# Kernel optimization log

Hardware: AMD Instinct MI355X
Metric: run time of the kernel (lower is better)

## Reference

```python
import jax, jax.numpy as jnp
import numpy as np

V = 6          # veldim
U = 4          # lstm_units
SEQLEN = 64
N = 1920 * 1080  # pixels in Lsx/Lsy


def setup_inputs() -> dict:
    key = jax.random.key(0)
    ks = jax.random.split(key, 24)
    f = lambda i, shape, s=0.1: jax.random.normal(ks[i], shape, jnp.float32) * s
    inp = {
        'vel': f(0, (V,), 1.0),
        'Lsx': jax.random.normal(ks[1], (N, V), jnp.float32),
        'Lsy': jax.random.normal(ks[2], (N, V), jnp.float32),
        # parameters (torch.Tensor uninitialized -> we use small randn)
        'Wix': f(3, (V, U)), 'Wih': f(4, (V * U, U)), 'bi': f(5, (V, U)),
        'Wfx': f(6, (V, U)), 'Wfh': f(7, (V * U, U)), 'bf': f(8, (V, U)),
        'Wox': f(9, (V, U)), 'Woh': f(10, (V * U, U)), 'bo': f(11, (V, U)),
        'Wgx': f(12, (V, U)), 'Wgh': f(13, (V * U, U)), 'bg': f(14, (V, U)),
        'linear': f(15, (V, U)), 'bl': f(16, (V,)),
        # initial hidden/cell state (torch.randn in init_hidden)
        'h0': jax.random.normal(ks[17], (V, U), jnp.float32),
        'c0': jax.random.normal(ks[18], (V, U), jnp.float32),
    }
    return inp


def reference(vel, Lsx, Lsy, Wix, Wih, bi, Wfx, Wfh, bf,
              Wox, Woh, bo, Wgx, Wgh, bg, linear, bl, h0, c0):
    def step(x, h, c):
        xv = x.reshape(V, 1)  # broadcast column, as x.view(6,1)
        # torch: sum(W * (R @ h), dim=1).view(V,U); row 4j+u of R@h is h[j]
        # => gate_h[j,u] = dot(W[4j+u,:], h[j,:])
        def gh(W):
            return jnp.einsum('juk,jk->ju', W.reshape(V, U, U), h)
        it = jax.nn.sigmoid(Wix * xv + gh(Wih) + bi)
        ft = jax.nn.sigmoid(Wfx * xv + gh(Wfh) + bf)
        ot = jax.nn.sigmoid(Wox * xv + gh(Woh) + bo)
        cbar = jax.nn.sigmoid(Wgx * xv + gh(Wgh) + bg)  # sigmoid, as in source
        c2 = ft * c + it * cbar
        h2 = ot * jax.nn.sigmoid(c2)  # sigmoid (not tanh), as in source
        out = jnp.tanh(jnp.sum(linear * h2, axis=1) + bl)  # (V,)
        return out, h2, c2

    out, h, c = step(vel, h0, c0)
    vels = out  # i == 0 branch

    # i = 1 .. seqlen-1: vels += previous out, then advance the cell.
    def body(carry, _):
        h, c, out, vels = carry
        vels = vels + out
        out, h, c = step(out, h, c)
        return (h, c, out, vels), None

    (h, c, out, vels), _ = jax.lax.scan(body, (h, c, out, vels), None,
                                        length=SEQLEN - 1)

    # f_hat = cat(sum(Lsx*vels,-1), sum(Lsy*vels,-1)) -> (N, 2)
    fx = Lsx @ vels
    fy = Lsy @ vels
    return jnp.stack([fx, fy], axis=-1)
```

## Files before the change

### kernel.cpp

```cpp
#include <hip/hip_runtime.h>
#include <hip/hip_bf16.h>


#define V 6
#define U 4
#define SEQLEN 64

__device__ __forceinline__ float sigm(float x) {
    return 1.0f / (1.0f + __expf(-x));
}
__device__ __forceinline__ float tanh_f(float x) {
    float e = __expf(2.0f * x);
    return 1.0f - 2.0f / (e + 1.0f);
}

template <int CTRL>
__device__ __forceinline__ float qp(float x) {
    return __int_as_float(
        __builtin_amdgcn_mov_dpp(__float_as_int(x), CTRL, 0xF, 0xF, true));
}

__global__ void lstm_vels_kernel(
    const float* __restrict__ vel,
    const float* __restrict__ Wix, const float* __restrict__ Wih, const float* __restrict__ bi,
    const float* __restrict__ Wfx, const float* __restrict__ Wfh, const float* __restrict__ bf_,
    const float* __restrict__ Wox, const float* __restrict__ Woh, const float* __restrict__ bo,
    const float* __restrict__ Wgx, const float* __restrict__ Wgh, const float* __restrict__ bg,
    const float* __restrict__ lin, const float* __restrict__ bl,
    const float* __restrict__ h0,  const float* __restrict__ c0,
    float* __restrict__ vels_out)
{
    const int lane = threadIdx.x;
    if (lane >= V * U) return;
    const int j  = lane >> 2;
    const int u  = lane & 3;
    const int r4 = lane * 4;

    const float wix = Wix[lane], bii = bi[lane];
    const float wfx = Wfx[lane], bff = bf_[lane];
    const float wox = Wox[lane], boo = bo[lane];
    const float wgx = Wgx[lane], bgg = bg[lane];
    const float li  = lin[lane];
    const float blj = bl[j];

    const int k1 = u ^ 1, k2 = u ^ 2, k3 = u ^ 3;
    const float wi0 = Wih[r4 + u],  wi1 = Wih[r4 + k1];
    const float wi2 = Wih[r4 + k2], wi3 = Wih[r4 + k3];
    const float wf0 = Wfh[r4 + u],  wf1 = Wfh[r4 + k1];
    const float wf2 = Wfh[r4 + k2], wf3 = Wfh[r4 + k3];
    const float wo0 = Woh[r4 + u],  wo1 = Woh[r4 + k1];
    const float wo2 = Woh[r4 + k2], wo3 = Woh[r4 + k3];
    const float wg0 = Wgh[r4 + u],  wg1 = Wgh[r4 + k1];
    const float wg2 = Wgh[r4 + k2], wg3 = Wgh[r4 + k3];

    float h = h0[lane];
    float c = c0[lane];
    float x = vel[j];

    float vels = 0.0f, o = 0.0f;

    for (int i = 0; i < SEQLEN; ++i) {
        if (i > 0) { vels += o; x = o; }

        const float hA = qp<0xB1>(h);
        const float hB = qp<0x4E>(h);
        const float hC = qp<0x4E>(hA);

        float pi = fmaf(wix, x, bii);
        pi = fmaf(wi0, h, pi); pi = fmaf(wi1, hA, pi);
        pi = fmaf(wi2, hB, pi); pi = fmaf(wi3, hC, pi);
        float pf = fmaf(wfx, x, bff);
        pf = fmaf(wf0, h, pf); pf = fmaf(wf1, hA, pf);
        pf = fmaf(wf2, hB, pf); pf = fmaf(wf3, hC, pf);
        float po = fmaf(wox, x, boo);
        po = fmaf(wo0, h, po); po = fmaf(wo1, hA, po);
        po = fmaf(wo2, hB, po); po = fmaf(wo3, hC, po);
        float pg = fmaf(wgx, x, bgg);
        pg = fmaf(wg0, h, pg); pg = fmaf(wg1, hA, pg);
        pg = fmaf(wg2, hB, pg); pg = fmaf(wg3, hC, pg);

        const float it = sigm(pi);
        const float ft = sigm(pf);
        const float ot = sigm(po);
        const float gt = sigm(pg);

        c = fmaf(ft, c, it * gt);
        h = ot * sigm(c);

        float s = li * h;
        s += qp<0xB1>(s);
        s += qp<0x4E>(s);
        o = tanh_f(s + blj);

        if (i == 0) vels = o;
    }

    if (u == 0) vels_out[j] = vels;
}

__global__ __launch_bounds__(256) void flow_kernel(
    const float* __restrict__ Lsx, const float* __restrict__ Lsy,
    const float* __restrict__ velsp, float* __restrict__ out, int n)
{
    const int t = blockIdx.x * blockDim.x + threadIdx.x;

    float v[6];
#pragma unroll
    for (int k = 0; k < 6; ++k) v[k] = velsp[k];

    const int p0 = t * 2;
    if (p0 + 1 < n) {
        const float4* ax = reinterpret_cast<const float4*>(Lsx + (size_t)p0 * 6);
        const float4* ay = reinterpret_cast<const float4*>(Lsy + (size_t)p0 * 6);
        union { float4 q[3]; float s[12]; } bx, by;
        bx.q[0] = ax[0]; bx.q[1] = ax[1]; bx.q[2] = ax[2];
        by.q[0] = ay[0]; by.q[1] = ay[1]; by.q[2] = ay[2];

        float4 r;
        float fx0 = 0.0f, fy0 = 0.0f, fx1 = 0.0f, fy1 = 0.0f;
#pragma unroll
        for (int k = 0; k < 6; ++k) {
            fx0 = fmaf(bx.s[k],     v[k], fx0);
            fy0 = fmaf(by.s[k],     v[k], fy0);
            fx1 = fmaf(bx.s[6 + k], v[k], fx1);
            fy1 = fmaf(by.s[6 + k], v[k], fy1);
        }
        r.x = fx0; r.y = fy0; r.z = fx1; r.w = fy1;
        reinterpret_cast<float4*>(out)[t] = r;
    } else {
        for (int p = p0; p < n; ++p) {
            float fx = 0.0f, fy = 0.0f;
            for (int k = 0; k < 6; ++k) {
                fx = fmaf(Lsx[(size_t)p * 6 + k], v[k], fx);
                fy = fmaf(Lsy[(size_t)p * 6 + k], v[k], fy);
            }
            out[2 * p]     = fx;
            out[2 * p + 1] = fy;
        }
    }
}

extern "C" void kernel_launch(void* const* d_in, const int* in_sizes, int n_in,
                              void* d_out, int out_size, void* d_ws, size_t ws_size,
                              hipStream_t stream)
{
    const float* vel  = (const float*)d_in[0];
    const float* Lsx  = (const float*)d_in[1];
    const float* Lsy  = (const float*)d_in[2];
    const float* Wix  = (const float*)d_in[3];
    const float* Wih  = (const float*)d_in[4];
    const float* bi   = (const float*)d_in[5];
    const float* Wfx  = (const float*)d_in[6];
    const float* Wfh  = (const float*)d_in[7];
    const float* bf_  = (const float*)d_in[8];
    const float* Wox  = (const float*)d_in[9];
    const float* Woh  = (const float*)d_in[10];
    const float* bo   = (const float*)d_in[11];
    const float* Wgx  = (const float*)d_in[12];
    const float* Wgh  = (const float*)d_in[13];
    const float* bg   = (const float*)d_in[14];
    const float* lin  = (const float*)d_in[15];
    const float* bl   = (const float*)d_in[16];
    const float* h0   = (const float*)d_in[17];
    const float* c0   = (const float*)d_in[18];

    float* vels = (float*)d_ws;
    const int n = in_sizes[1] / V;

    lstm_vels_kernel<<<1, 64, 0, stream>>>(vel, Wix, Wih, bi, Wfx, Wfh, bf_,
                                           Wox, Woh, bo, Wgx, Wgh, bg,
                                           lin, bl, h0, c0, vels);

    const int nt = (n + 1) / 2;
    flow_kernel<<<(nt + 255) / 256, 256, 0, stream>>>(Lsx, Lsy, vels,
                                                      (float*)d_out, n);
}
```

Measured before the change: 176.7 us.

## Fuse LSTM recurrence into flow kernel with grid-stride loop

```diff
diff --git a/kernel.cpp b/kernel.cpp
--- a/kernel.cpp
+++ b/kernel.cpp
@@ -20,7 +20,7 @@
         __builtin_amdgcn_mov_dpp(__float_as_int(x), CTRL, 0xF, 0xF, true));
 }
 
-__global__ void lstm_vels_kernel(
+__global__ __launch_bounds__(256, 4) void fused_lstm_flow_kernel(
     const float* __restrict__ vel,
     const float* __restrict__ Wix, const float* __restrict__ Wih, const float* __restrict__ bi,
     const float* __restrict__ Wfx, const float* __restrict__ Wfh, const float* __restrict__ bf_,
@@ -28,115 +28,122 @@
     const float* __restrict__ Wgx, const float* __restrict__ Wgh, const float* __restrict__ bg,
     const float* __restrict__ lin, const float* __restrict__ bl,
     const float* __restrict__ h0,  const float* __restrict__ c0,
-    float* __restrict__ vels_out)
+    const float* __restrict__ Lsx, const float* __restrict__ Lsy,
+    float* __restrict__ out, int n)
 {
-    const int lane = threadIdx.x;
-    if (lane >= V * U) return;
-    const int j  = lane >> 2;
-    const int u  = lane & 3;
-    const int r4 = lane * 4;
+    __shared__ float vels_s[8];
 
-    const float wix = Wix[lane], bii = bi[lane];
-    const float wfx = Wfx[lane], bff = bf_[lane];
-    const float wox = Wox[lane], boo = bo[lane];
-    const float wgx = Wgx[lane], bgg = bg[lane];
-    const float li  = lin[lane];
-    const float blj = bl[j];
+    if (threadIdx.x < 24) {
+        const int lane = threadIdx.x;
+        const int j  = lane >> 2;
+        const int u  = lane & 3;
+        const int r4 = lane * 4;
 
-    const int k1 = u ^ 1, k2 = u ^ 2, k3 = u ^ 3;
-    const float wi0 = Wih[r4 + u],  wi1 = Wih[r4 + k1];
-    const float wi2 = Wih[r4 + k2], wi3 = Wih[r4 + k3];
-    const float wf0 = Wfh[r4 + u],  wf1 = Wfh[r4 + k1];
-    const float wf2 = Wfh[r4 + k2], wf3 = Wfh[r4 + k3];
-    const float wo0 = Woh[r4 + u],  wo1 = Woh[r4 + k1];
-    const float wo2 = Woh[r4 + k2], wo3 = Woh[r4 + k3];
-    const float wg0 = Wgh[r4 + u],  wg1 = Wgh[r4 + k1];
-    const float wg2 = Wgh[r4 + k2], wg3 = Wgh[r4 + k3];
+        const float wix = Wix[lane], bii = bi[lane];
+        const float wfx = Wfx[lane], bff = bf_[lane];
+        const float wox = Wox[lane], boo = bo[lane];
+        const float wgx = Wgx[lane], bgg = bg[lane];
+        const float li  = lin[lane];
+        const float blj = bl[j];
 
-    float h = h0[lane];
-    float c = c0[lane];
-    float x = vel[j];
+        const int k1 = u ^ 1, k2 = u ^ 2, k3 = u ^ 3;
+        const float wi0 = Wih[r4 + u],  wi1 = Wih[r4 + k1];
+        const float wi2 = Wih[r4 + k2], wi3 = Wih[r4 + k3];
+        const float wf0 = Wfh[r4 + u],  wf1 = Wfh[r4 + k1];
+        const float wf2 = Wfh[r4 + k2], wf3 = Wfh[r4 + k3];
+        const float wo0 = Woh[r4 + u],  wo1 = Woh[r4 + k1];
+        const float wo2 = Woh[r4 + k2], wo3 = Woh[r4 + k3];
+        const float wg0 = Wgh[r4 + u],  wg1 = Wgh[r4 + k1];
+        const float wg2 = Wgh[r4 + k2], wg3 = Wgh[r4 + k3];
 
-    float vels = 0.0f, o = 0.0f;
+        float h = h0[lane];
+        float c = c0[lane];
+        float x = vel[j];
 
-    for (int i = 0; i < SEQLEN; ++i) {
-        if (i > 0) { vels += o; x = o; }
+        float vels = 0.0f, o = 0.0f;
 
-        const float hA = qp<0xB1>(h);
-        const float hB = qp<0x4E>(h);
-        const float hC = qp<0x4E>(hA);
+        for (int i = 0; i < SEQLEN; ++i) {
+            if (i > 0) { vels += o; x = o; }
 
-        float pi = fmaf(wix, x, bii);
-        pi = fmaf(wi0, h, pi); pi = fmaf(wi1, hA, pi);
-        pi = fmaf(wi2, hB, pi); pi = fmaf(wi3, hC, pi);
-        float pf = fmaf(wfx, x, bff);
-        pf = fmaf(wf0, h, pf); pf = fmaf(wf1, hA, pf);
-        pf = fmaf(wf2, hB, pf); pf = fmaf(wf3, hC, pf);
-        float po = fmaf(wox, x, boo);
-        po = fmaf(wo0, h, po); po = fmaf(wo1, hA, po);
-        po = fmaf(wo2, hB, po); po = fmaf(wo3, hC, po);
-        float pg = fmaf(wgx, x, bgg);
-        pg = fmaf(wg0, h, pg); pg = fmaf(wg1, hA, pg);
-        pg = fmaf(wg2, hB, pg); pg = fmaf(wg3, hC, pg);
+            const float hA = qp<0xB1>(h);
+            const float hB = qp<0x4E>(h);
+            const float hC = qp<0x4E>(hA);
 
-        const float it = sigm(pi);
-        const float ft = sigm(pf);
-        const float ot = sigm(po);
-        const float gt = sigm(pg);
+            float pi = fmaf(wix, x, bii);
+            pi = fmaf(wi0, h, pi); pi = fmaf(wi1, hA, pi);
+            pi = fmaf(wi2, hB, pi); pi = fmaf(wi3, hC, pi);
+            float pf = fmaf(wfx, x, bff);
+            pf = fmaf(wf0, h, pf); pf = fmaf(wf1, hA, pf);
+            pf = fmaf(wf2, hB, pf); pf = fmaf(wf3, hC, pf);
+            float po = fmaf(wox, x, boo);
+            po = fmaf(wo0, h, po); po = fmaf(wo1, hA, po);
+            po = fmaf(wo2, hB, po); po = fmaf(wo3, hC, po);
+            float pg = fmaf(wgx, x, bgg);
+            pg = fmaf(wg0, h, pg); pg = fmaf(wg1, hA, pg);
+            pg = fmaf(wg2, hB, pg); pg = fmaf(wg3, hC, pg);
 
-        c = fmaf(ft, c, it * gt);
-        h = ot * sigm(c);
+            const float it = sigm(pi);
+            const float ft = sigm(pf);
+            const float ot = sigm(po);
+            const float gt = sigm(pg);
 
-        float s = li * h;
-        s += qp<0xB1>(s);
-        s += qp<0x4E>(s);
-        o = tanh_f(s + blj);
+            c = fmaf(ft, c, it * gt);
+            h = ot * sigm(c);
 
-        if (i == 0) vels = o;
+            float s = li * h;
+            s += qp<0xB1>(s);
+            s += qp<0x4E>(s);
+            o = tanh_f(s + blj);
+
+            if (i == 0) vels = o;
+        }
+
+        if (u == 0) vels_s[j] = vels;
     }
 
-    if (u == 0) vels_out[j] = vels;
-}
+    __syncthreads();
 
-__global__ __launch_bounds__(256) void flow_kernel(
-    const float* __restrict__ Lsx, const float* __restrict__ Lsy,
-    const float* __restrict__ velsp, float* __restrict__ out, int n)
-{
-    const int t = blockIdx.x * blockDim.x + threadIdx.x;
+    const float v0 = vels_s[0], v1 = vels_s[1], v2 = vels_s[2];
+    const float v3 = vels_s[3], v4 = vels_s[4], v5 = vels_s[5];
 
-    float v[6];
-#pragma unroll
-    for (int k = 0; k < 6; ++k) v[k] = velsp[k];
+    const int nt = n >> 1;
+    const int stride = gridDim.x * blockDim.x;
 
-    const int p0 = t * 2;
-    if (p0 + 1 < n) {
-        const float4* ax = reinterpret_cast<const float4*>(Lsx + (size_t)p0 * 6);
-        const float4* ay = reinterpret_cast<const float4*>(Lsy + (size_t)p0 * 6);
+    for (int tp = blockIdx.x * blockDim.x + threadIdx.x; tp < nt; tp += stride) {
+        const float4* ax = reinterpret_cast<const float4*>(Lsx + (size_t)tp * 12);
+        const float4* ay = reinterpret_cast<const float4*>(Lsy + (size_t)tp * 12);
         union { float4 q[3]; float s[12]; } bx, by;
         bx.q[0] = ax[0]; bx.q[1] = ax[1]; bx.q[2] = ax[2];
         by.q[0] = ay[0]; by.q[1] = ay[1]; by.q[2] = ay[2];
 
+        float fx0 = bx.s[0] * v0, fy0 = by.s[0] * v0;
+        float fx1 = bx.s[6] * v0, fy1 = by.s[6] * v0;
+        fx0 = fmaf(bx.s[1],  v1, fx0); fy0 = fmaf(by.s[1],  v1, fy0);
+        fx1 = fmaf(bx.s[7],  v1, fx1); fy1 = fmaf(by.s[7],  v1, fy1);
+        fx0 = fmaf(bx.s[2],  v2, fx0); fy0 = fmaf(by.s[2],  v2, fy0);
+        fx1 = fmaf(bx.s[8],  v2, fx1); fy1 = fmaf(by.s[8],  v2, fy1);
+        fx0 = fmaf(bx.s[3],  v3, fx0); fy0 = fmaf(by.s[3],  v3, fy0);
+        fx1 = fmaf(bx.s[9],  v3, fx1); fy1 = fmaf(by.s[9],  v3, fy1);
+        fx0 = fmaf(bx.s[4],  v4, fx0); fy0 = fmaf(by.s[4],  v4, fy0);
+        fx1 = fmaf(bx.s[10], v4, fx1); fy1 = fmaf(by.s[10], v4, fy1);
+        fx0 = fmaf(bx.s[5],  v5, fx0); fy0 = fmaf(by.s[5],  v5, fy0);
+        fx1 = fmaf(bx.s[11], v5, fx1); fy1 = fmaf(by.s[11], v5, fy1);
+
         float4 r;
-        float fx0 = 0.0f, fy0 = 0.0f, fx1 = 0.0f, fy1 = 0.0f;
-#pragma unroll
+        r.x = fx0; r.y = fy0; r.z = fx1; r.w = fy1;
+        reinterpret_cast<float4*>(out)[tp] = r;
+    }
+
+    if ((n & 1) && blockIdx.x == 0 && threadIdx.x == 0) {
+        const int p = n - 1;
+        float fx = 0.0f, fy = 0.0f;
+        const float vv[6] = {v0, v1, v2, v3, v4, v5};
         for (int k = 0; k < 6; ++k) {
-            fx0 = fmaf(bx.s[k],     v[k], fx0);
-            fy0 = fmaf(by.s[k],     v[k], fy0);
-            fx1 = fmaf(bx.s[6 + k], v[k], fx1);
-            fy1 = fmaf(by.s[6 + k], v[k], fy1);
+            fx = fmaf(Lsx[(size_t)p * 6 + k], vv[k], fx);
+            fy = fmaf(Lsy[(size_t)p * 6 + k], vv[k], fy);
         }
-        r.x = fx0; r.y = fy0; r.z = fx1; r.w = fy1;
-        reinterpret_cast<float4*>(out)[t] = r;
-    } else {
-        for (int p = p0; p < n; ++p) {
-            float fx = 0.0f, fy = 0.0f;
-            for (int k = 0; k < 6; ++k) {
-                fx = fmaf(Lsx[(size_t)p * 6 + k], v[k], fx);
-                fy = fmaf(Lsy[(size_t)p * 6 + k], v[k], fy);
-            }
-            out[2 * p]     = fx;
-            out[2 * p + 1] = fy;
-        }
+        out[2 * p]     = fx;
+        out[2 * p + 1] = fy;
     }
 }
 
@@ -164,14 +171,10 @@
     const float* h0   = (const float*)d_in[17];
     const float* c0   = (const float*)d_in[18];
 
-    float* vels = (float*)d_ws;
     const int n = in_sizes[1] / V;
 
-    lstm_vels_kernel<<<1, 64, 0, stream>>>(vel, Wix, Wih, bi, Wfx, Wfh, bf_,
-                                           Wox, Woh, bo, Wgx, Wgh, bg,
-                                           lin, bl, h0, c0, vels);
-
-    const int nt = (n + 1) / 2;
-    flow_kernel<<<(nt + 255) / 256, 256, 0, stream>>>(Lsx, Lsy, vels,
-                                                      (float*)d_out, n);
+    const int nblocks = 1024;
+    fused_lstm_flow_kernel<<<nblocks, 256, 0, stream>>>(
+        vel, Wix, Wih, bi, Wfx, Wfh, bf_, Wox, Woh, bo, Wgx, Wgh, bg,
+        lin, bl, h0, c0, Lsx, Lsy, (float*)d_out, n);
 }
```

New measurement: 173.9 us. No clear change (-1.5%).
